# Kernel optimization log

Hardware: AMD Instinct MI355X
Metric: run time of the kernel (lower is better)

## Reference

```python
import jax, jax.numpy as jnp
import numpy as np

EPS = 1e-5

def setup_inputs() -> dict:
    key = jax.random.key(0)
    ks = jax.random.split(key, 9)
    N, D, L, C = 1, 128, 256, 256
    OC, PC = 32, 256
    msa_matrix = jax.random.normal(ks[0], (N, D, L, C), dtype=jnp.float32)
    ln_w = jnp.ones((C,), dtype=jnp.float32)
    ln_b = jnp.zeros((C,), dtype=jnp.float32)
    s = 1.0 / np.sqrt(C)
    Wl = jax.random.uniform(ks[1], (OC, C), dtype=jnp.float32, minval=-s, maxval=s)
    bl = jax.random.uniform(ks[2], (OC,), dtype=jnp.float32, minval=-s, maxval=s)
    Wr = jax.random.uniform(ks[3], (OC, C), dtype=jnp.float32, minval=-s, maxval=s)
    br = jax.random.uniform(ks[4], (OC,), dtype=jnp.float32, minval=-s, maxval=s)
    so = 1.0 / np.sqrt(OC * OC)
    Wout = jax.random.uniform(ks[5], (PC, OC * OC), dtype=jnp.float32, minval=-so, maxval=so)
    bout = jax.random.uniform(ks[6], (PC,), dtype=jnp.float32, minval=-so, maxval=so)
    return {"msa_matrix": msa_matrix, "ln_w": ln_w, "ln_b": ln_b,
            "Wl": Wl, "bl": bl, "Wr": Wr, "br": br, "Wout": Wout, "bout": bout}

def reference(msa_matrix, ln_w, ln_b, Wl, bl, Wr, br, Wout, bout):
    N, D, L, C = msa_matrix.shape
    OC = Wl.shape[0]
    # LayerNorm over channels
    mu = jnp.mean(msa_matrix, axis=-1, keepdims=True)
    var = jnp.var(msa_matrix, axis=-1, keepdims=True)
    x = (msa_matrix - mu) * jax.lax.rsqrt(var + EPS) * ln_w + ln_b
    # Dual projections: [N, D, L, OC]
    left = jnp.einsum('ndlc,oc->ndlo', x, Wl) + bl
    right = (jnp.einsum('ndlc,oc->ndlo', x, Wr) + br) / D
    # Outer-product mean over MSA depth: [N, L, L, OC, OC]
    outprod = jnp.einsum('ndlc,ndmq->nlmcq', left, right)
    outprod = outprod.reshape(N, L, L, OC * OC)
    # Output projection to pair channels
    return jnp.einsum('nlmk,pk->nlmp', outprod, Wout) + bout
```

## Files before the change

### kernel.cpp

```cpp
#include <hip/hip_runtime.h>

#define EPS 1e-5f

static constexpr int D  = 128;
static constexpr int L  = 256;
static constexpr int C  = 256;
static constexpr int OC = 32;
static constexpr int PC = 256;

typedef __attribute__((ext_vector_type(8))) short bfrag8;
typedef __attribute__((ext_vector_type(4))) short bhalf4;
typedef __attribute__((ext_vector_type(4))) float f32x4;

__device__ inline unsigned short f2bf(float f) {
  union { float f; unsigned u; } v; v.f = f;
  unsigned r = v.u + 0x7FFF + ((v.u >> 16) & 1);
  return (unsigned short)(r >> 16);
}

__global__ __launch_bounds__(256)
void prep(const float* __restrict__ Wl, const float* __restrict__ Wr,
          const float* __restrict__ Wout,
          unsigned short* __restrict__ Wbf3, unsigned short* __restrict__ Wlnf) {
  const int t = threadIdx.x, b = blockIdx.x;
  {
    const int e0 = (b * 256 + t) * 4;
    const int lane = (e0 >> 3) & 63, ks = (e0 >> 9) & 31, pf = e0 >> 14;
    const int p = pf * 16 + (lane & 15);
    unsigned short v[4];
    #pragma unroll
    for (int j = 0; j < 4; ++j) {
      const int kp = ks * 32 + ((lane >> 4) * 8) + ((e0 + j) & 7);
      const int c = kp & 31, q = kp >> 5;
      v[j] = f2bf(Wout[p * 1024 + c * 32 + q]);
    }
    *(bhalf4*)(Wbf3 + e0) = *(bhalf4*)v;
  }
  if (b < 16) {
    const int e0 = (b * 256 + t) * 4;
    const int lane = (e0 >> 3) & 63, ks = (e0 >> 9) & 7, nf = e0 >> 12;
    const int n = nf * 16 + (lane & 15);
    unsigned short v[4];
    #pragma unroll
    for (int j = 0; j < 4; ++j) {
      const int k = ks * 32 + ((lane >> 4) * 8) + ((e0 + j) & 7);
      v[j] = f2bf(n < 32 ? Wl[n * 256 + k] : Wr[(n - 32) * 256 + k]);
    }
    *(bhalf4*)(Wlnf + e0) = *(bhalf4*)v;
  }
}

__global__ __launch_bounds__(256, 4)
void ln_proj(const float* __restrict__ msa,
             const float* __restrict__ lnw, const float* __restrict__ lnb,
             const unsigned short* __restrict__ Wlnf,
             const float* __restrict__ bl, const float* __restrict__ br,
             unsigned short* __restrict__ leftT, unsigned short* __restrict__ rightT) {
  __shared__ char xb[32768];

  const int t = threadIdx.x, lane = t & 63, w = t >> 6;
  const int d0 = blockIdx.x * 8, l0 = blockIdx.y * 8;

  float4 xv[16];
  #pragma unroll
  for (int i = 0; i < 16; ++i) {
    const int r = i * 4 + w, dd = r & 7, ll = r >> 3;
    xv[i] = *(const float4*)(msa + ((size_t)(d0 + dd) * 256 + (l0 + ll)) * 256 + lane * 4);
  }

  float mu[16], rs[16];
  #pragma unroll
  for (int i = 0; i < 16; ++i) {
    float s  = xv[i].x + xv[i].y + xv[i].z + xv[i].w;
    float s2 = xv[i].x * xv[i].x + xv[i].y * xv[i].y + xv[i].z * xv[i].z + xv[i].w * xv[i].w;
    #pragma unroll
    for (int off = 32; off >= 1; off >>= 1) {
      s  += __shfl_xor(s, off);
      s2 += __shfl_xor(s2, off);
    }
    mu[i] = s * (1.0f / C);
    rs[i] = rsqrtf(s2 * (1.0f / C) - mu[i] * mu[i] + EPS);
  }

  {
    const float4 wv = *(const float4*)(lnw + lane * 4);
    const float4 bv = *(const float4*)(lnb + lane * 4);
    #pragma unroll
    for (int i = 0; i < 16; ++i) {
      const int r = i * 4 + w;
      float4 v = xv[i];
      unsigned short u[4];
      u[0] = f2bf((v.x - mu[i]) * rs[i] * wv.x + bv.x);
      u[1] = f2bf((v.y - mu[i]) * rs[i] * wv.y + bv.y);
      u[2] = f2bf((v.z - mu[i]) * rs[i] * wv.z + bv.z);
      u[3] = f2bf((v.w - mu[i]) * rs[i] * wv.w + bv.w);
      *(bhalf4*)&xb[r * 512 + ((lane * 8) ^ ((r & 7) << 4))] = *(bhalf4*)u;
    }
  }
  __syncthreads();

  bfrag8 wf[8];
  {
    const unsigned short* Wp = Wlnf + ((size_t)w * 8 * 64 + lane) * 8;
    #pragma unroll
    for (int ks = 0; ks < 8; ++ks) wf[ks] = *(const bfrag8*)(Wp + ks * 512);
  }
  f32x4 acc[4];
  #pragma unroll
  for (int mf = 0; mf < 4; ++mf) acc[mf] = (f32x4)0.f;
  #pragma unroll
  for (int ks = 0; ks < 8; ++ks) {
    #pragma unroll
    for (int mf = 0; mf < 4; ++mf) {
      const int row = mf * 16 + (lane & 15);
      const bfrag8 af = *(const bfrag8*)&xb[row * 512 +
                          ((ks * 64 + ((lane >> 4) << 4)) ^ ((row & 7) << 4))];
      acc[mf] = __builtin_amdgcn_mfma_f32_16x16x32_bf16(af, wf[ks], acc[mf], 0, 0, 0);
    }
  }

  {
    const int n = w * 16 + (lane & 15);
    const int side = n >> 5, o = n & 31;
    const float bias = side ? br[o] : bl[o];
    const float sc = side ? (1.0f / D) : 1.0f;
    unsigned short* dst = side ? rightT : leftT;
    #pragma unroll
    for (int mf = 0; mf < 4; ++mf) {
      const int rbase = mf * 16 + ((lane >> 4) << 2);
      const int ll = rbase >> 3, ddb = rbase & 7;
      unsigned short u[4];
      #pragma unroll
      for (int r = 0; r < 4; ++r) u[r] = f2bf((acc[mf][r] + bias) * sc);
      *(bhalf4*)(dst + ((size_t)(l0 + ll) * 32 + o) * 128 + d0 + ddb) = *(bhalf4*)u;
    }
  }
}

__global__ __launch_bounds__(512, 4)
void fused_mfma(const unsigned short* __restrict__ leftT,
                const unsigned short* __restrict__ rightT,
                const unsigned short* __restrict__ Wbf3,
                const float* __restrict__ bout,
                float* __restrict__ out) {
  __shared__ char smem[65536];

  const int flat = blockIdx.x;
  const int wg = (flat & 7) * 256 + (flat >> 3);
  const int mt = wg & 31, lt = wg >> 5;
  const int l0 = lt * 4, m0 = mt * 8;

  const char* Aslab = (const char*)(leftT  + (size_t)l0 * 32 * 128);
  const char* Bslab = (const char*)(rightT + (size_t)m0 * 32 * 128);

  const int tid = threadIdx.x, lane = tid & 63, w = tid >> 6;
  const int wr = w >> 2, wc = w & 3;

  f32x4 acc[4][4];
  #pragma unroll
  for (int i = 0; i < 4; ++i)
    #pragma unroll
    for (int j = 0; j < 4; ++j) acc[i][j] = (f32x4)0.f;

  for (int kh = 0; kh < 2; ++kh) {
    #pragma unroll
    for (int i = 0; i < 2; ++i) {
      const int lb = (i * 512 + tid) * 16;
      const int row = lb >> 7;
      const int sb = (lb & 127) ^ ((row & 7) << 4);
      __builtin_amdgcn_global_load_lds((const void*)(Aslab + (size_t)row * 256 + kh * 128 + sb),
                                       (void*)&smem[lb], 16, 0, 0);
    }
    #pragma unroll
    for (int i = 0; i < 4; ++i) {
      const int lb = (i * 512 + tid) * 16;
      const int row = lb >> 7;
      const int sb = (lb & 127) ^ ((row & 7) << 4);
      __builtin_amdgcn_global_load_lds((const void*)(Bslab + (size_t)row * 256 + kh * 128 + sb),
                                       (void*)&smem[16384 + lb], 16, 0, 0);
    }
    __syncthreads();
    #pragma unroll
    for (int ks = 0; ks < 2; ++ks) {
      const int kb = ks * 64 + ((lane >> 4) << 4);
      bfrag8 a[4], b[4];
      #pragma unroll
      for (int i = 0; i < 4; ++i) {
        const int row = wr * 64 + i * 16 + (lane & 15);
        a[i] = *(const bfrag8*)&smem[(row << 7) + (kb ^ ((row & 7) << 4))];
      }
      #pragma unroll
      for (int j = 0; j < 4; ++j) {
        const int row = wc * 64 + j * 16 + (lane & 15);
        b[j] = *(const bfrag8*)&smem[16384 + (row << 7) + (kb ^ ((row & 7) << 4))];
      }
      #pragma unroll
      for (int i = 0; i < 4; ++i)
        #pragma unroll
        for (int j = 0; j < 4; ++j)
          acc[i][j] = __builtin_amdgcn_mfma_f32_16x16x32_bf16(a[i], b[j], acc[i][j], 0, 0, 0);
    }
    __syncthreads();
  }

  {
    #pragma unroll
    for (int i = 0; i < 4; ++i) {
      const int rowb = wr * 64 + i * 16 + ((lane >> 4) << 2);
      const int ll = rowb >> 5, cc = rowb & 31;
      #pragma unroll
      for (int j = 0; j < 4; ++j) {
        const int col = wc * 64 + j * 16 + (lane & 15);
        const int mm = col >> 5, q = col & 31;
        const int pair = ll * 8 + mm;
        const int kp = q * 32 + cc;
        const int S = (pair & 7) ^ ((q >> 1) & 7);
        const int byte = pair * 2048 + ((kp * 2) ^ (S << 4));
        uint2 u;
        u.x = (unsigned)f2bf(acc[i][j][0]) | ((unsigned)f2bf(acc[i][j][1]) << 16);
        u.y = (unsigned)f2bf(acc[i][j][2]) | ((unsigned)f2bf(acc[i][j][3]) << 16);
        *(uint2*)&smem[byte] = u;
      }
    }
  }
  __syncthreads();

  f32x4 oacc[2][2];
  #pragma unroll
  for (int u = 0; u < 2; ++u)
    #pragma unroll
    for (int pj = 0; pj < 2; ++pj) oacc[u][pj] = (f32x4)0.f;

  #pragma unroll 2
  for (int ks = 0; ks < 32; ++ks) {
    bfrag8 wf[2], osf[2];
    #pragma unroll
    for (int u = 0; u < 2; ++u) {
      const int pf = w * 2 + u;
      wf[u] = *(const bfrag8*)(Wbf3 + (((size_t)pf * 32 + ks) * 64 + lane) * 8);
    }
    #pragma unroll
    for (int pj = 0; pj < 2; ++pj) {
      const int pair = pj * 16 + (lane & 15);
      const int S = (pair & 7) ^ ((ks >> 1) & 7);
      const int byte = pair * 2048 + ((ks * 64 + ((lane >> 4) << 4)) ^ (S << 4));
      osf[pj] = *(const bfrag8*)&smem[byte];
    }
    #pragma unroll
    for (int u = 0; u < 2; ++u)
      #pragma unroll
      for (int pj = 0; pj < 2; ++pj)
        oacc[u][pj] = __builtin_amdgcn_mfma_f32_16x16x32_bf16(wf[u], osf[pj], oacc[u][pj], 0, 0, 0);
  }

  {
    #pragma unroll
    for (int u = 0; u < 2; ++u) {
      const int p0 = (w * 2 + u) * 16 + ((lane >> 4) << 2);
      const float4 bb = *(const float4*)&bout[p0];
      #pragma unroll
      for (int pj = 0; pj < 2; ++pj) {
        const int pair = pj * 16 + (lane & 15);
        const int ll = pair >> 3, mm = pair & 7;
        float4 v;
        v.x = oacc[u][pj][0] + bb.x;
        v.y = oacc[u][pj][1] + bb.y;
        v.z = oacc[u][pj][2] + bb.z;
        v.w = oacc[u][pj][3] + bb.w;
        *(float4*)&out[((size_t)(l0 + ll) * L + (m0 + mm)) * PC + p0] = v;
      }
    }
  }
}

extern "C" void kernel_launch(void* const* d_in, const int* in_sizes, int n_in,
                              void* d_out, int out_size, void* d_ws, size_t ws_size,
                              hipStream_t stream) {
  const float* msa  = (const float*)d_in[0];
  const float* ln_w = (const float*)d_in[1];
  const float* ln_b = (const float*)d_in[2];
  const float* Wl   = (const float*)d_in[3];
  const float* bl   = (const float*)d_in[4];
  const float* Wr   = (const float*)d_in[5];
  const float* br   = (const float*)d_in[6];
  const float* Wout = (const float*)d_in[7];
  const float* bout = (const float*)d_in[8];
  float* out = (float*)d_out;

  unsigned short* leftT  = (unsigned short*)d_ws;
  unsigned short* rightT = leftT + (size_t)L * 32 * 128;
  unsigned short* Wbf3   = rightT + (size_t)L * 32 * 128;
  unsigned short* Wlnf   = Wbf3 + (size_t)PC * 1024;

  prep<<<dim3(256), 256, 0, stream>>>(Wl, Wr, Wout, Wbf3, Wlnf);
  ln_proj<<<dim3(16, 32), 256, 0, stream>>>(msa, ln_w, ln_b, Wlnf, bl, br, leftT, rightT);
  fused_mfma<<<dim3(2048), 512, 0, stream>>>(leftT, rightT, Wbf3, bout, out);
}
```

Before: 89.45 us.

## Overlap staging of second K-half with first compute and double-buffer output GEMM loads

```diff
diff --git a/kernel.cpp b/kernel.cpp
--- a/kernel.cpp
+++ b/kernel.cpp
@@ -162,15 +162,17 @@
     #pragma unroll
     for (int j = 0; j < 4; ++j) acc[i][j] = (f32x4)0.f;
 
-  for (int kh = 0; kh < 2; ++kh) {
+  auto stageA = [&](int kh, int dst) {
     #pragma unroll
     for (int i = 0; i < 2; ++i) {
       const int lb = (i * 512 + tid) * 16;
       const int row = lb >> 7;
       const int sb = (lb & 127) ^ ((row & 7) << 4);
       __builtin_amdgcn_global_load_lds((const void*)(Aslab + (size_t)row * 256 + kh * 128 + sb),
-                                       (void*)&smem[lb], 16, 0, 0);
-    }
+                                       (void*)&smem[dst + lb], 16, 0, 0);
+    }
+  };
+  auto stageB = [&](int kh) {
     #pragma unroll
     for (int i = 0; i < 4; ++i) {
       const int lb = (i * 512 + tid) * 16;
@@ -179,7 +181,8 @@
       __builtin_amdgcn_global_load_lds((const void*)(Bslab + (size_t)row * 256 + kh * 128 + sb),
                                        (void*)&smem[16384 + lb], 16, 0, 0);
     }
-    __syncthreads();
+  };
+  auto computeKh = [&](int abase) {
     #pragma unroll
     for (int ks = 0; ks < 2; ++ks) {
       const int kb = ks * 64 + ((lane >> 4) << 4);
@@ -187,21 +190,33 @@
       #pragma unroll
       for (int i = 0; i < 4; ++i) {
         const int row = wr * 64 + i * 16 + (lane & 15);
-        a[i] = *(const bfrag8*)&smem[(row << 7) + (kb ^ ((row & 7) << 4))];
+        a[i] = *(const bfrag8*)&smem[abase + (row << 7) + (kb ^ ((row & 7) << 4))];
       }
       #pragma unroll
       for (int j = 0; j < 4; ++j) {
         const int row = wc * 64 + j * 16 + (lane & 15);
         b[j] = *(const bfrag8*)&smem[16384 + (row << 7) + (kb ^ ((row & 7) << 4))];
       }
+      __builtin_amdgcn_s_setprio(1);
       #pragma unroll
       for (int i = 0; i < 4; ++i)
         #pragma unroll
         for (int j = 0; j < 4; ++j)
           acc[i][j] = __builtin_amdgcn_mfma_f32_16x16x32_bf16(a[i], b[j], acc[i][j], 0, 0, 0);
-    }
-    __syncthreads();
-  }
+      __builtin_amdgcn_s_setprio(0);
+    }
+  };
+
+  stageA(0, 0);
+  stageB(0);
+  __syncthreads();
+  stageA(1, 49152);
+  computeKh(0);
+  __syncthreads();
+  stageB(1);
+  __syncthreads();
+  computeKh(49152);
+  __syncthreads();
 
   {
     #pragma unroll
@@ -231,26 +246,44 @@
     #pragma unroll
     for (int pj = 0; pj < 2; ++pj) oacc[u][pj] = (f32x4)0.f;
 
-  #pragma unroll 2
-  for (int ks = 0; ks < 32; ++ks) {
-    bfrag8 wf[2], osf[2];
-    #pragma unroll
-    for (int u = 0; u < 2; ++u) {
-      const int pf = w * 2 + u;
-      wf[u] = *(const bfrag8*)(Wbf3 + (((size_t)pf * 32 + ks) * 64 + lane) * 8);
-    }
+  const unsigned short* wp0 = Wbf3 + (((size_t)(w * 2)     * 32) * 64 + lane) * 8;
+  const unsigned short* wp1 = Wbf3 + (((size_t)(w * 2 + 1) * 32) * 64 + lane) * 8;
+
+  auto ldos = [&](int ks, bfrag8* o) {
     #pragma unroll
     for (int pj = 0; pj < 2; ++pj) {
       const int pair = pj * 16 + (lane & 15);
       const int S = (pair & 7) ^ ((ks >> 1) & 7);
-      const int byte = pair * 2048 + ((ks * 64 + ((lane >> 4) << 4)) ^ (S << 4));
-      osf[pj] = *(const bfrag8*)&smem[byte];
-    }
-    #pragma unroll
-    for (int u = 0; u < 2; ++u)
-      #pragma unroll
-      for (int pj = 0; pj < 2; ++pj)
-        oacc[u][pj] = __builtin_amdgcn_mfma_f32_16x16x32_bf16(wf[u], osf[pj], oacc[u][pj], 0, 0, 0);
+      o[pj] = *(const bfrag8*)&smem[pair * 2048 + ((ks * 64 + ((lane >> 4) << 4)) ^ (S << 4))];
+    }
+  };
+
+  bfrag8 wfA0 = *(const bfrag8*)(wp0);
+  bfrag8 wfA1 = *(const bfrag8*)(wp1);
+  bfrag8 osA[2]; ldos(0, osA);
+  bfrag8 wfB0, wfB1, osB[2];
+
+  for (int ks = 0; ks < 32; ks += 2) {
+    wfB0 = *(const bfrag8*)(wp0 + (ks + 1) * 512);
+    wfB1 = *(const bfrag8*)(wp1 + (ks + 1) * 512);
+    ldos(ks + 1, osB);
+    __builtin_amdgcn_s_setprio(1);
+    oacc[0][0] = __builtin_amdgcn_mfma_f32_16x16x32_bf16(wfA0, osA[0], oacc[0][0], 0, 0, 0);
+    oacc[0][1] = __builtin_amdgcn_mfma_f32_16x16x32_bf16(wfA0, osA[1], oacc[0][1], 0, 0, 0);
+    oacc[1][0] = __builtin_amdgcn_mfma_f32_16x16x32_bf16(wfA1, osA[0], oacc[1][0], 0, 0, 0);
+    oacc[1][1] = __builtin_amdgcn_mfma_f32_16x16x32_bf16(wfA1, osA[1], oacc[1][1], 0, 0, 0);
+    __builtin_amdgcn_s_setprio(0);
+    if (ks + 2 < 32) {
+      wfA0 = *(const bfrag8*)(wp0 + (ks + 2) * 512);
+      wfA1 = *(const bfrag8*)(wp1 + (ks + 2) * 512);
+      ldos(ks + 2, osA);
+    }
+    __builtin_amdgcn_s_setprio(1);
+    oacc[0][0] = __builtin_amdgcn_mfma_f32_16x16x32_bf16(wfB0, osB[0], oacc[0][0], 0, 0, 0);
+    oacc[0][1] = __builtin_amdgcn_mfma_f32_16x16x32_bf16(wfB0, osB[1], oacc[0][1], 0, 0, 0);
+    oacc[1][0] = __builtin_amdgcn_mfma_f32_16x16x32_bf16(wfB1, osB[0], oacc[1][0], 0, 0, 0);
+    oacc[1][1] = __builtin_amdgcn_mfma_f32_16x16x32_bf16(wfB1, osB[1], oacc[1][1], 0, 0, 0);
+    __builtin_amdgcn_s_setprio(0);
   }
 
   {
```

Result: faster. 86.50 us (-3.3%).

## Double-buffer A staging and prefetch Wout fragments in a register ring

Applied to the files above, without the earlier changes.

```diff
diff --git a/kernel.cpp b/kernel.cpp
--- a/kernel.cpp
+++ b/kernel.cpp
@@ -162,15 +162,17 @@
     #pragma unroll
     for (int j = 0; j < 4; ++j) acc[i][j] = (f32x4)0.f;
 
-  for (int kh = 0; kh < 2; ++kh) {
+  auto stageA = [&](int kh, int dst) {
     #pragma unroll
     for (int i = 0; i < 2; ++i) {
       const int lb = (i * 512 + tid) * 16;
       const int row = lb >> 7;
       const int sb = (lb & 127) ^ ((row & 7) << 4);
       __builtin_amdgcn_global_load_lds((const void*)(Aslab + (size_t)row * 256 + kh * 128 + sb),
-                                       (void*)&smem[lb], 16, 0, 0);
-    }
+                                       (void*)&smem[dst + lb], 16, 0, 0);
+    }
+  };
+  auto stageB = [&](int kh) {
     #pragma unroll
     for (int i = 0; i < 4; ++i) {
       const int lb = (i * 512 + tid) * 16;
@@ -179,7 +181,8 @@
       __builtin_amdgcn_global_load_lds((const void*)(Bslab + (size_t)row * 256 + kh * 128 + sb),
                                        (void*)&smem[16384 + lb], 16, 0, 0);
     }
-    __syncthreads();
+  };
+  auto computeKh = [&](int abase) {
     #pragma unroll
     for (int ks = 0; ks < 2; ++ks) {
       const int kb = ks * 64 + ((lane >> 4) << 4);
@@ -187,7 +190,7 @@
       #pragma unroll
       for (int i = 0; i < 4; ++i) {
         const int row = wr * 64 + i * 16 + (lane & 15);
-        a[i] = *(const bfrag8*)&smem[(row << 7) + (kb ^ ((row & 7) << 4))];
+        a[i] = *(const bfrag8*)&smem[abase + (row << 7) + (kb ^ ((row & 7) << 4))];
       }
       #pragma unroll
       for (int j = 0; j < 4; ++j) {
@@ -200,8 +203,18 @@
         for (int j = 0; j < 4; ++j)
           acc[i][j] = __builtin_amdgcn_mfma_f32_16x16x32_bf16(a[i], b[j], acc[i][j], 0, 0, 0);
     }
-    __syncthreads();
-  }
+  };
+
+  stageA(0, 0);
+  stageB(0);
+  __syncthreads();
+  stageA(1, 49152);
+  computeKh(0);
+  __syncthreads();
+  stageB(1);
+  __syncthreads();
+  computeKh(49152);
+  __syncthreads();
 
   {
     #pragma unroll
@@ -223,6 +236,16 @@
       }
     }
   }
+
+  const unsigned short* wp0 = Wbf3 + (((size_t)(w * 2)     * 32) * 64 + lane) * 8;
+  const unsigned short* wp1 = Wbf3 + (((size_t)(w * 2 + 1) * 32) * 64 + lane) * 8;
+
+  bfrag8 wfs[4][2];
+  #pragma unroll
+  for (int s = 0; s < 4; ++s) {
+    wfs[s][0] = *(const bfrag8*)(wp0 + s * 512);
+    wfs[s][1] = *(const bfrag8*)(wp1 + s * 512);
+  }
   __syncthreads();
 
   f32x4 oacc[2][2];
@@ -231,26 +254,25 @@
     #pragma unroll
     for (int pj = 0; pj < 2; ++pj) oacc[u][pj] = (f32x4)0.f;
 
-  #pragma unroll 2
+  #pragma unroll
   for (int ks = 0; ks < 32; ++ks) {
-    bfrag8 wf[2], osf[2];
-    #pragma unroll
-    for (int u = 0; u < 2; ++u) {
-      const int pf = w * 2 + u;
-      wf[u] = *(const bfrag8*)(Wbf3 + (((size_t)pf * 32 + ks) * 64 + lane) * 8);
-    }
+    bfrag8 osf[2];
     #pragma unroll
     for (int pj = 0; pj < 2; ++pj) {
       const int pair = pj * 16 + (lane & 15);
       const int S = (pair & 7) ^ ((ks >> 1) & 7);
-      const int byte = pair * 2048 + ((ks * 64 + ((lane >> 4) << 4)) ^ (S << 4));
-      osf[pj] = *(const bfrag8*)&smem[byte];
-    }
-    #pragma unroll
-    for (int u = 0; u < 2; ++u)
-      #pragma unroll
-      for (int pj = 0; pj < 2; ++pj)
-        oacc[u][pj] = __builtin_amdgcn_mfma_f32_16x16x32_bf16(wf[u], osf[pj], oacc[u][pj], 0, 0, 0);
+      osf[pj] = *(const bfrag8*)&smem[pair * 2048 +
+                  ((ks * 64 + ((lane >> 4) << 4)) ^ (S << 4))];
+    }
+    const int s = ks & 3;
+    oacc[0][0] = __builtin_amdgcn_mfma_f32_16x16x32_bf16(wfs[s][0], osf[0], oacc[0][0], 0, 0, 0);
+    oacc[0][1] = __builtin_amdgcn_mfma_f32_16x16x32_bf16(wfs[s][0], osf[1], oacc[0][1], 0, 0, 0);
+    oacc[1][0] = __builtin_amdgcn_mfma_f32_16x16x32_bf16(wfs[s][1], osf[0], oacc[1][0], 0, 0, 0);
+    oacc[1][1] = __builtin_amdgcn_mfma_f32_16x16x32_bf16(wfs[s][1], osf[1], oacc[1][1], 0, 0, 0);
+    if (ks + 4 < 32) {
+      wfs[s][0] = *(const bfrag8*)(wp0 + (ks + 4) * 512);
+      wfs[s][1] = *(const bfrag8*)(wp1 + (ks + 4) * 512);
+    }
   }
 
   {
```

Measured after the change: 91.12 us. Within noise of the previous version (+1.9%).
